# Kernel optimization log

Measured on AMD Instinct MI355X. Metric: run time of the kernel, lower is better.

Reference implementation:

```python
import jax, jax.numpy as jnp
import numpy as np

V = 50000      # word vocab
CV = 63        # char vocab (60 chars + 3 tags)
HW = 512       # word hidden size
HC = 256       # char hidden size
NLW = 2        # word lstm layers
NLC = 2        # char lstm layers
L = 12         # chars in the word


def _lstm_layers(x, H, C, Wih, Whh, bih, bhh):
    """One time-step of a multi-layer LSTM (PyTorch gate order i,f,g,o).
    x: [1, D], H/C: [nl, 1, D]. Returns (top_h, newH, newC)."""
    nl = Wih.shape[0]
    newH, newC = [], []
    inp = x
    for l in range(nl):
        gates = inp @ Wih[l].T + H[l] @ Whh[l].T + bih[l] + bhh[l]  # [1, 4D]
        i, f, g, o = jnp.split(gates, 4, axis=-1)
        i = jax.nn.sigmoid(i)
        f = jax.nn.sigmoid(f)
        g = jnp.tanh(g)
        o = jax.nn.sigmoid(o)
        c = f * C[l] + i * g
        h = o * jnp.tanh(c)
        newH.append(h)
        newC.append(c)
        inp = h
    return inp, jnp.stack(newH), jnp.stack(newC)


def setup_inputs() -> dict:
    key = jax.random.key(0)
    ks = jax.random.split(key, 20)
    sW = 1.0 / np.sqrt(HW)
    sC = 1.0 / np.sqrt(HC)
    return {
        "x_word": jax.random.randint(ks[0], (1,), 0, V),
        "x_char": jax.random.randint(ks[1], (L,), 0, CV),
        "h_word_h": jax.random.normal(ks[2], (NLW, 1, HW), jnp.float32),
        "h_word_c": jax.random.normal(ks[3], (NLW, 1, HW), jnp.float32),
        "h_char_h": jax.random.normal(ks[4], (NLC, 1, HC), jnp.float32),
        "h_char_c": jax.random.normal(ks[5], (NLC, 1, HC), jnp.float32),
        "word_emb": jax.random.normal(ks[6], (V, HW), jnp.float32),
        "word_Wih": jax.random.normal(ks[7], (NLW, 4 * HW, HW), jnp.float32) * sW,
        "word_Whh": jax.random.normal(ks[8], (NLW, 4 * HW, HW), jnp.float32) * sW,
        "word_bih": jax.random.normal(ks[9], (NLW, 4 * HW), jnp.float32) * sW,
        "word_bhh": jax.random.normal(ks[10], (NLW, 4 * HW), jnp.float32) * sW,
        "dec_W": jax.random.normal(ks[11], (V, HW), jnp.float32) * sW,
        "dec_b": jax.random.normal(ks[12], (V,), jnp.float32) * sW,
        "char_emb": jax.random.normal(ks[13], (CV, HC), jnp.float32),
        "char_Wih": jax.random.normal(ks[14], (NLC, 4 * HC, HC), jnp.float32) * sC,
        "char_Whh": jax.random.normal(ks[15], (NLC, 4 * HC, HC), jnp.float32) * sC,
        "char_bih": jax.random.normal(ks[16], (NLC, 4 * HC), jnp.float32) * sC,
        "char_bhh": jax.random.normal(ks[17], (NLC, 4 * HC), jnp.float32) * sC,
        "char_to_embedding": jax.random.normal(ks[18], (HW, HC), jnp.float32),
        "g_w": jax.random.normal(ks[19], (HW,), jnp.float32) * sW,
        "g_b": jax.random.normal(jax.random.fold_in(key, 99), (1,), jnp.float32),
    }


def reference(x_word, x_char, h_word_h, h_word_c, h_char_h, h_char_c,
              word_emb, word_Wih, word_Whh, word_bih, word_bhh,
              dec_W, dec_b,
              char_emb, char_Wih, char_Whh, char_bih, char_bhh,
              char_to_embedding, g_w, g_b):
    # character-level recurrence over the word's characters
    def char_step(carry, cidx):
        H, C = carry
        xc = char_emb[cidx][None, :]  # [1, HC]
        _, H, C = _lstm_layers(xc, H, C, char_Wih, char_Whh, char_bih, char_bhh)
        return (H, C), None

    (h_char_h, h_char_c), _ = jax.lax.scan(char_step, (h_char_h, h_char_c), x_char)

    # note: original uses h_char[1] (the CELL state) of the last layer
    x_c = char_to_embedding @ h_char_c[-1].T          # [HW, 1]
    x_w = word_emb[x_word[0]][None, :]                # [1, HW]
    g = jax.nn.relu(jnp.dot(g_w, x_w[0]) + g_b[0])    # scalar gate
    x = (1.0 - g) * x_w + g * x_c.T                   # [1, HW]

    y, h_word_h, h_word_c = _lstm_layers(x, h_word_h, h_word_c,
                                         word_Wih, word_Whh, word_bih, word_bhh)
    y = y @ dec_W.T + dec_b                           # [1, V]
    return y, h_word_h, h_word_c, h_char_h, h_char_c
```

## Files before the change

kernel.cpp:

```cpp
#include <hip/hip_runtime.h>
#include <stdint.h>


#define SCOPE_AGT __HIP_MEMORY_SCOPE_AGENT

#define CNT_CHAR   0
#define CNT_CDONE  64
#define CNT_MIX    128
#define CNT_W0     192
#define CNT_W1     256

static __device__ __forceinline__ float dot4(float4 w, const float* p){
    return w.x*p[0] + w.y*p[1] + w.z*p[2] + w.w*p[3];
}
static __device__ __forceinline__ float dot44(float4 a, float4 b){
    return a.x*b.x + a.y*b.y + a.z*b.z + a.w*b.w;
}
static __device__ __forceinline__ float sigf(float x){ return 1.0f / (1.0f + __expf(-x)); }
static __device__ __forceinline__ float tanhf_(float x){
    x = fminf(fmaxf(x, -15.0f), 15.0f);
    float e = __expf(2.0f * x);
    return (e - 1.0f) / (e + 1.0f);
}

static __device__ __forceinline__ float gload(const float* p){
    return __hip_atomic_load(p, __ATOMIC_RELAXED, SCOPE_AGT);
}
static __device__ __forceinline__ void gstore(float* p, float v){
    __hip_atomic_store(p, v, __ATOMIC_RELAXED, SCOPE_AGT);
}
static __device__ __forceinline__ void bar_add(int* c){
    __hip_atomic_fetch_add(c, 1, __ATOMIC_RELAXED, SCOPE_AGT);
}
static __device__ __forceinline__ void bar_wait_fast(int* c, int tgt){
    while (__hip_atomic_load(c, __ATOMIC_RELAXED, SCOPE_AGT) < tgt)
        __builtin_amdgcn_s_sleep(2);
}
static __device__ __forceinline__ void bar_wait_slow(int* c, int tgt){
    while (__hip_atomic_load(c, __ATOMIC_RELAXED, SCOPE_AGT) < tgt)
        __builtin_amdgcn_s_sleep(64);
}

static __device__ __forceinline__ void dec_prefetch(const float* __restrict__ dec_W,
        int start, int stride, int lane){
    float acc[8] = {0.f,0.f,0.f,0.f,0.f,0.f,0.f,0.f};
    for (int r = start; r < 50000; r += 8*stride){
        #pragma unroll
        for (int k = 0; k < 8; ++k){
            int rr = r + k * stride;
            if (rr < 50000) acc[k] += dec_W[(size_t)rr * 512 + lane * 8];
        }
    }
    float s = acc[0]+acc[1]+acc[2]+acc[3]+acc[4]+acc[5]+acc[6]+acc[7];
    asm volatile("" :: "v"(s));
}

__global__ __launch_bounds__(256, 2) void k_fused(
    const int* __restrict__ x_word, const int* __restrict__ x_char,
    const float* __restrict__ hwh, const float* __restrict__ hwc,
    const float* __restrict__ hch, const float* __restrict__ hcc,
    const float* __restrict__ word_emb,
    const float* __restrict__ wWih, const float* __restrict__ wWhh,
    const float* __restrict__ wbih, const float* __restrict__ wbhh,
    const float* __restrict__ dec_W, const float* __restrict__ dec_b,
    const float* __restrict__ char_emb,
    const float* __restrict__ cWih, const float* __restrict__ cWhh,
    const float* __restrict__ cbih, const float* __restrict__ cbhh,
    const float* __restrict__ cte,
    const float* __restrict__ g_w, const float* __restrict__ g_b,
    float* __restrict__ ws, float* __restrict__ out)
{
    const int tid  = threadIdx.x;
    const int bx   = blockIdx.x;
    const int lane = tid & 63;
    const int wv   = tid >> 6;
    int* cnt = (int*)(ws + 4096);

    if (bx < 64){
        __shared__ float sH1[256], sH2[256], sE[256], sg1[16], sg2[16];
        float* h1b = ws;
        float* h2b = ws + 512;

        const int rg = tid >> 4, lane16 = tid & 15;
        const int gate = rg & 3, uu = rg >> 2;
        const int u = (bx << 2) + uu;
        const int row = (gate << 8) + u, row2 = 1024 + row;

        float4 w1i[4], w1h[4], w2i[4], w2h[4];
        {
            const float4* p1i = (const float4*)(cWih + (size_t)row  * 256) + lane16 * 4;
            const float4* p1h = (const float4*)(cWhh + (size_t)row  * 256) + lane16 * 4;
            const float4* p2i = (const float4*)(cWih + (size_t)row2 * 256) + lane16 * 4;
            const float4* p2h = (const float4*)(cWhh + (size_t)row2 * 256) + lane16 * 4;
            #pragma unroll
            for (int j = 0; j < 4; ++j){ w1i[j]=p1i[j]; w1h[j]=p1h[j]; w2i[j]=p2i[j]; w2h[j]=p2h[j]; }
        }
        const float b1 = cbih[row]  + cbhh[row];
        const float b2 = cbih[row2] + cbhh[row2];

        float c1r = 0.f, c2r = 0.f, h1fin = 0.f, h2fin = 0.f;
        if (tid < 4)      c1r = hcc[(bx<<2) + tid];
        else if (tid < 8) c2r = hcc[256 + (bx<<2) + (tid-4)];

        for (int t = 0; t <= 12; ++t){
            sH1[tid] = (t == 0) ? hch[tid] : gload(h1b + (t & 1)*256 + tid);
            if (t >= 1) sH2[tid] = (t == 1) ? hch[256 + tid]
                                            : gload(h2b + ((t-1) & 1)*256 + tid);
            if (t < 12) sE[tid] = char_emb[x_char[t]*256 + tid];
            __syncthreads();

            float a1 = 0.f, a2 = 0.f;
            if (t < 12){
                const float* xp = sE  + lane16*16;
                const float* hp = sH1 + lane16*16;
                #pragma unroll
                for (int j = 0; j < 4; ++j) a1 += dot4(w1i[j], xp + 4*j) + dot4(w1h[j], hp + 4*j);
            }
            if (t >= 1){
                const float* xp = sH1 + lane16*16;
                const float* hp = sH2 + lane16*16;
                #pragma unroll
                for (int j = 0; j < 4; ++j) a2 += dot4(w2i[j], xp + 4*j) + dot4(w2h[j], hp + 4*j);
            }
            #pragma unroll
            for (int m = 8; m >= 1; m >>= 1){
                a1 += __shfl_xor(a1, m, 64);
                a2 += __shfl_xor(a2, m, 64);
            }
            if (lane16 == 0){
                if (t < 12) sg1[rg] = a1 + b1;
                if (t >= 1) sg2[rg] = a2 + b2;
            }
            __syncthreads();

            if (tid < 4){
                if (t < 12){
                    int uh = (bx << 2) + tid;
                    float gi = sigf(sg1[tid*4+0]);
                    float gf = sigf(sg1[tid*4+1]);
                    float gg = tanhf_(sg1[tid*4+2]);
                    float go = sigf(sg1[tid*4+3]);
                    float c = gf * c1r + gi * gg;
                    c1r = c;
                    float h = go * tanhf_(c);
                    h1fin = h;
                    gstore(h1b + ((t+1) & 1)*256 + uh, h);
                }
            } else if (tid < 8){
                if (t >= 1){
                    int q = tid - 4;
                    int uh = (bx << 2) + q;
                    float gi = sigf(sg2[q*4+0]);
                    float gf = sigf(sg2[q*4+1]);
                    float gg = tanhf_(sg2[q*4+2]);
                    float go = sigf(sg2[q*4+3]);
                    float c = gf * c2r + gi * gg;
                    c2r = c;
                    float h = go * tanhf_(c);
                    h2fin = h;
                    if (t < 12) gstore(h2b + (t & 1)*256 + uh, h);
                    else        gstore(ws + 1280 + uh, c);
                }
            }
            __syncthreads();
            if (tid == 0){
                bar_add(&cnt[CNT_CHAR]);
                if (t < 12) bar_wait_fast(&cnt[CNT_CHAR], 64*(t+1));
            }
            __syncthreads();
        }
        if (tid == 0) bar_add(&cnt[CNT_CDONE]);

        if (tid < 4){
            int uh = (bx << 2) + tid;
            out[52048 + uh] = h1fin;
            out[52560 + uh] = c1r;
        } else if (tid < 8){
            int uh = (bx << 2) + (tid - 4);
            out[52048 + 256 + uh] = h2fin;
            out[52560 + 256 + uh] = c2r;
        }

    } else if (bx < 192){
        __shared__ float sC2[256];
        __shared__ float sXCW[512];
        __shared__ float sMisc[8];
        const int vw = ((bx - 64) << 2) + wv;
        float4 wi0[4], wi1[4], wh0[4], wh1[4]; float bs[4];
        #pragma unroll
        for (int gq = 0; gq < 4; ++gq){
            const size_t rf = (size_t)((gq << 9) + vw);
            const float4* pi = (const float4*)(wWih + rf*512) + lane*2;
            const float4* ph = (const float4*)(wWhh + rf*512) + lane*2;
            wi0[gq] = pi[0]; wi1[gq] = pi[1];
            wh0[gq] = ph[0]; wh1[gq] = ph[1];
            bs[gq] = wbih[rf] + wbhh[rf];
        }
        const float4* hv = (const float4*)(hwh) + lane*2;
        const float4 hva = hv[0], hvb = hv[1];
        const size_t wbase = (size_t)x_word[0] * 512;
        const float4* wep = (const float4*)(word_emb + wbase) + lane*2;
        const float4 wea = wep[0], web = wep[1];

        if (bx == 64){
            float p = g_w[2*tid]   * word_emb[wbase + 2*tid]
                    + g_w[2*tid+1] * word_emb[wbase + 2*tid+1];
            #pragma unroll
            for (int m = 32; m >= 1; m >>= 1) p += __shfl_xor(p, m, 64);
            if (lane == 0) sMisc[wv] = p;
            __syncthreads();
            if (tid == 0)
                gstore(ws + 3072, fmaxf(sMisc[0]+sMisc[1]+sMisc[2]+sMisc[3] + g_b[0], 0.0f));
        }

        dec_prefetch(dec_W, ((bx - 64) << 2) + wv, 1024, lane);

        if (tid == 0) bar_wait_slow(&cnt[CNT_CDONE], 64);
        __syncthreads();
        sC2[tid] = gload(ws + 1280 + tid);
        __syncthreads();

        {
            float4 cv  = ((const float4*)(cte + (size_t)vw*256))[lane];
            float4 c2v = ((const float4*)sC2)[lane];
            float acc = dot44(cv, c2v);
            #pragma unroll
            for (int m = 32; m >= 1; m >>= 1) acc += __shfl_xor(acc, m, 64);
            if (lane == 0) gstore(ws + 1536 + vw, acc);
        }
        __syncthreads();
        if (tid == 0){ bar_add(&cnt[CNT_MIX]); bar_wait_fast(&cnt[CNT_MIX], 128); }
        __syncthreads();
        sXCW[tid]       = gload(ws + 1536 + tid);
        sXCW[256 + tid] = gload(ws + 1536 + 256 + tid);
        if (tid == 0) sMisc[4] = gload(ws + 3072);
        __syncthreads();

        {
            const float g  = sMisc[4];
            const float og = 1.0f - g;
            const float4 x0 = ((const float4*)sXCW)[lane*2];
            const float4 x1 = ((const float4*)sXCW)[lane*2 + 1];
            float4 xa, xb;
            xa.x = og*wea.x + g*x0.x; xa.y = og*wea.y + g*x0.y;
            xa.z = og*wea.z + g*x0.z; xa.w = og*wea.w + g*x0.w;
            xb.x = og*web.x + g*x1.x; xb.y = og*web.y + g*x1.y;
            xb.z = og*web.z + g*x1.z; xb.w = og*web.w + g*x1.w;
            float ac[4];
            #pragma unroll
            for (int gq = 0; gq < 4; ++gq){
                float a = dot44(wi0[gq], xa) + dot44(wi1[gq], xb)
                        + dot44(wh0[gq], hva) + dot44(wh1[gq], hvb);
                #pragma unroll
                for (int m = 32; m >= 1; m >>= 1) a += __shfl_xor(a, m, 64);
                ac[gq] = a;
            }
            if (lane == 0){
                float gi = sigf(ac[0] + bs[0]);
                float gf = sigf(ac[1] + bs[1]);
                float gg = tanhf_(ac[2] + bs[2]);
                float go = sigf(ac[3] + bs[3]);
                float c = gf * hwc[vw] + gi * gg;
                float h = go * tanhf_(c);
                gstore(ws + 2048 + vw, h);
                out[50000 + vw] = h;
                out[51024 + vw] = c;
            }
        }
        __syncthreads();
        if (tid == 0) bar_add(&cnt[CNT_W0]);

    } else {
        __shared__ float sX1[512];
        const int vw = ((bx - 192) << 2) + wv;
        float4 wi0[4], wi1[4], wh0[4], wh1[4]; float bs[4];
        #pragma unroll
        for (int gq = 0; gq < 4; ++gq){
            const size_t rf = (size_t)(2048 + (gq << 9) + vw);
            const float4* pi = (const float4*)(wWih + rf*512) + lane*2;
            const float4* ph = (const float4*)(wWhh + rf*512) + lane*2;
            wi0[gq] = pi[0]; wi1[gq] = pi[1];
            wh0[gq] = ph[0]; wh1[gq] = ph[1];
            bs[gq] = wbih[rf] + wbhh[rf];
        }
        const float4* hv = (const float4*)(hwh + 512) + lane*2;
        const float4 hva = hv[0], hvb = hv[1];

        dec_prefetch(dec_W, 512 + ((bx - 192) << 2) + wv, 1024, lane);

        if (tid == 0) bar_wait_slow(&cnt[CNT_W0], 128);
        __syncthreads();
        sX1[tid]       = gload(ws + 2048 + tid);
        sX1[256 + tid] = gload(ws + 2048 + 256 + tid);
        __syncthreads();
        {
            const float4 xa = ((const float4*)sX1)[lane*2];
            const float4 xb = ((const float4*)sX1)[lane*2 + 1];
            float ac[4];
            #pragma unroll
            for (int gq = 0; gq < 4; ++gq){
                float a = dot44(wi0[gq], xa) + dot44(wi1[gq], xb)
                        + dot44(wh0[gq], hva) + dot44(wh1[gq], hvb);
                #pragma unroll
                for (int m = 32; m >= 1; m >>= 1) a += __shfl_xor(a, m, 64);
                ac[gq] = a;
            }
            if (lane == 0){
                float gi = sigf(ac[0] + bs[0]);
                float gf = sigf(ac[1] + bs[1]);
                float gg = tanhf_(ac[2] + bs[2]);
                float go = sigf(ac[3] + bs[3]);
                float c = gf * hwc[512 + vw] + gi * gg;
                float h = go * tanhf_(c);
                gstore(ws + 2560 + vw, h);
                out[50000 + 512 + vw] = h;
                out[51024 + 512 + vw] = c;
            }
        }
        __syncthreads();
        if (tid == 0) bar_add(&cnt[CNT_W1]);
    }

    __shared__ float sHW[512];
    if (tid == 0) bar_wait_slow(&cnt[CNT_W1], 128);
    __syncthreads();
    sHW[tid]       = gload(ws + 2560 + tid);
    sHW[256 + tid] = gload(ws + 2560 + 256 + tid);
    __syncthreads();
    {
        const float4 ha = ((const float4*)sHW)[lane*2];
        const float4 hb = ((const float4*)sHW)[lane*2 + 1];
        const int wid = (bx << 2) + wv;
        int r = wid;
        float4 a0 = make_float4(0,0,0,0), b0 = a0;
        if (r < 50000){
            const float4* wp = (const float4*)(dec_W + (size_t)r*512) + lane*2;
            a0 = wp[0]; b0 = wp[1];
        }
        while (r < 50000){
            const int rn = r + 1280;
            float4 a1 = make_float4(0,0,0,0), b1 = a1;
            if (rn < 50000){
                const float4* wp = (const float4*)(dec_W + (size_t)rn*512) + lane*2;
                a1 = wp[0]; b1 = wp[1];
            }
            float acc = dot44(a0, ha) + dot44(b0, hb);
            #pragma unroll
            for (int m = 32; m >= 1; m >>= 1) acc += __shfl_xor(acc, m, 64);
            if (lane == 0) out[r] = acc + dec_b[r];
            r = rn; a0 = a1; b0 = b1;
        }
    }
}

extern "C" void kernel_launch(void* const* d_in, const int* in_sizes, int n_in,
                              void* d_out, int out_size, void* d_ws, size_t ws_size,
                              hipStream_t stream)
{
    const int*   x_word   = (const int*)d_in[0];
    const int*   x_char   = (const int*)d_in[1];
    const float* hwh      = (const float*)d_in[2];
    const float* hwc      = (const float*)d_in[3];
    const float* hch      = (const float*)d_in[4];
    const float* hcc      = (const float*)d_in[5];
    const float* word_emb = (const float*)d_in[6];
    const float* wWih     = (const float*)d_in[7];
    const float* wWhh     = (const float*)d_in[8];
    const float* wbih     = (const float*)d_in[9];
    const float* wbhh     = (const float*)d_in[10];
    const float* dec_W    = (const float*)d_in[11];
    const float* dec_b    = (const float*)d_in[12];
    const float* char_emb = (const float*)d_in[13];
    const float* cWih     = (const float*)d_in[14];
    const float* cWhh     = (const float*)d_in[15];
    const float* cbih     = (const float*)d_in[16];
    const float* cbhh     = (const float*)d_in[17];
    const float* cte      = (const float*)d_in[18];
    const float* g_w      = (const float*)d_in[19];
    const float* g_b      = (const float*)d_in[20];

    float* ws  = (float*)d_ws;
    float* out = (float*)d_out;

    hipMemsetAsync((void*)((char*)d_ws + 16384), 0, 2048, stream);

    hipLaunchKernelGGL(k_fused, dim3(320), dim3(256), 0, stream,
        x_word, x_char, hwh, hwc, hch, hcc, word_emb,
        wWih, wWhh, wbih, wbhh, dec_W, dec_b,
        char_emb, cWih, cWhh, cbih, cbhh, cte, g_w, g_b,
        ws, out);
}
```

Measured before the change: 331.0 us.

## Replace atomic-counter barriers with per-block flags and widen decoder GEMV per wave

Global atomic-counter barriers between the char LSTM steps and word LSTM stages are replaced by per-block sequence flags polled by a full wavefront using ballot. Char-layer hidden states are exchanged through packed per-block slots read with 64-bit loads. The decoder projection now processes 8 rows per wave with 8 lanes per row and deeper unrolled loads, reducing shuffle-reduction overhead. This aims to cut barrier latency in the serial recurrence and to improve memory-level parallelism in the bandwidth-bound decoder. The cost is more polling traffic and relaxed-ordering assumptions on the flag/data visibility.

```diff
diff --git a/kernel.cpp b/kernel.cpp
--- a/kernel.cpp
+++ b/kernel.cpp
@@ -3,12 +3,7 @@
 
 
 #define SCOPE_AGT __HIP_MEMORY_SCOPE_AGENT
-
-#define CNT_CHAR   0
-#define CNT_CDONE  64
-#define CNT_MIX    128
-#define CNT_W0     192
-#define CNT_W1     256
+#define ALL64 0xFFFFFFFFFFFFFFFFull
 
 static __device__ __forceinline__ float dot4(float4 w, const float* p){
     return w.x*p[0] + w.y*p[1] + w.z*p[2] + w.w*p[3];
@@ -29,16 +24,17 @@
 static __device__ __forceinline__ void gstore(float* p, float v){
     __hip_atomic_store(p, v, __ATOMIC_RELAXED, SCOPE_AGT);
 }
-static __device__ __forceinline__ void bar_add(int* c){
-    __hip_atomic_fetch_add(c, 1, __ATOMIC_RELAXED, SCOPE_AGT);
-}
-static __device__ __forceinline__ void bar_wait_fast(int* c, int tgt){
-    while (__hip_atomic_load(c, __ATOMIC_RELAXED, SCOPE_AGT) < tgt)
-        __builtin_amdgcn_s_sleep(2);
-}
-static __device__ __forceinline__ void bar_wait_slow(int* c, int tgt){
-    while (__hip_atomic_load(c, __ATOMIC_RELAXED, SCOPE_AGT) < tgt)
-        __builtin_amdgcn_s_sleep(64);
+static __device__ __forceinline__ int gload_i(const int* p){
+    return __hip_atomic_load(p, __ATOMIC_RELAXED, SCOPE_AGT);
+}
+static __device__ __forceinline__ void gstore_i(int* p, int v){
+    __hip_atomic_store(p, v, __ATOMIC_RELAXED, SCOPE_AGT);
+}
+static __device__ __forceinline__ unsigned long long gload_ll(const float* p){
+    return __hip_atomic_load((const unsigned long long*)p, __ATOMIC_RELAXED, SCOPE_AGT);
+}
+static __device__ __forceinline__ unsigned long long gload_ll_i(const int* p){
+    return __hip_atomic_load((const unsigned long long*)p, __ATOMIC_RELAXED, SCOPE_AGT);
 }
 
 static __device__ __forceinline__ void dec_prefetch(const float* __restrict__ dec_W,
@@ -74,12 +70,17 @@
     const int bx   = blockIdx.x;
     const int lane = tid & 63;
     const int wv   = tid >> 6;
-    int* cnt = (int*)(ws + 4096);
+    int*   ws_i  = (int*)(ws + 4096);
+    int*   seqf  = ws_i;
+    int*   w0f   = ws_i + 128;
+    int*   w1f   = ws_i + 256;
+    int*   cdone = ws_i + 512;
+    float* fdata = ws + 4864;
+
+    __shared__ float sHW[512];
 
     if (bx < 64){
         __shared__ float sH1[256], sH2[256], sE[256], sg1[16], sg2[16];
-        float* h1b = ws;
-        float* h2b = ws + 512;
 
         const int rg = tid >> 4, lane16 = tid & 15;
         const int gate = rg & 3, uu = rg >> 2;
@@ -103,9 +104,31 @@
         else if (tid < 8) c2r = hcc[256 + (bx<<2) + (tid-4)];
 
         for (int t = 0; t <= 12; ++t){
-            sH1[tid] = (t == 0) ? hch[tid] : gload(h1b + (t & 1)*256 + tid);
-            if (t >= 1) sH2[tid] = (t == 1) ? hch[256 + tid]
-                                            : gload(h2b + ((t-1) & 1)*256 + tid);
+            if (t == 0){
+                sH1[tid] = hch[tid];
+            } else {
+                if (t == 1) sH2[tid] = hch[256 + tid];
+                if (tid < 64){
+                    const int p = (t - 1) & 1;
+                    const int* sq = seqf + p*64;
+                    while (true){
+                        int v = gload_i(sq + tid);
+                        if (__ballot(v >= t) == ALL64) break;
+                    }
+                    const float* dl = fdata + (size_t)(p*64 + tid)*16;
+                    union { unsigned long long u; float f[2]; } q0,q1,q2,q3;
+                    q0.u = gload_ll(dl + 0);
+                    q1.u = gload_ll(dl + 2);
+                    q2.u = gload_ll(dl + 4);
+                    q3.u = gload_ll(dl + 6);
+                    sH1[4*tid+0] = q0.f[0]; sH1[4*tid+1] = q0.f[1];
+                    sH1[4*tid+2] = q1.f[0]; sH1[4*tid+3] = q1.f[1];
+                    if (t >= 2){
+                        sH2[4*tid+0] = q2.f[0]; sH2[4*tid+1] = q2.f[1];
+                        sH2[4*tid+2] = q3.f[0]; sH2[4*tid+3] = q3.f[1];
+                    }
+                }
+            }
             if (t < 12) sE[tid] = char_emb[x_char[t]*256 + tid];
             __syncthreads();
 
@@ -133,9 +156,10 @@
             }
             __syncthreads();
 
+            const int p2 = t & 1;
+            float* dst = fdata + (size_t)(p2*64 + bx)*16;
             if (tid < 4){
                 if (t < 12){
-                    int uh = (bx << 2) + tid;
                     float gi = sigf(sg1[tid*4+0]);
                     float gf = sigf(sg1[tid*4+1]);
                     float gg = tanhf_(sg1[tid*4+2]);
@@ -144,12 +168,11 @@
                     c1r = c;
                     float h = go * tanhf_(c);
                     h1fin = h;
-                    gstore(h1b + ((t+1) & 1)*256 + uh, h);
+                    gstore(dst + tid, h);
                 }
             } else if (tid < 8){
                 if (t >= 1){
                     int q = tid - 4;
-                    int uh = (bx << 2) + q;
                     float gi = sigf(sg2[q*4+0]);
                     float gf = sigf(sg2[q*4+1]);
                     float gg = tanhf_(sg2[q*4+2]);
@@ -158,18 +181,13 @@
                     c2r = c;
                     float h = go * tanhf_(c);
                     h2fin = h;
-                    if (t < 12) gstore(h2b + (t & 1)*256 + uh, h);
-                    else        gstore(ws + 1280 + uh, c);
+                    if (t < 12) gstore(dst + 4 + q, h);
+                    else        gstore(ws + 1280 + (bx<<2) + q, c);
                 }
             }
             __syncthreads();
-            if (tid == 0){
-                bar_add(&cnt[CNT_CHAR]);
-                if (t < 12) bar_wait_fast(&cnt[CNT_CHAR], 64*(t+1));
-            }
-            __syncthreads();
-        }
-        if (tid == 0) bar_add(&cnt[CNT_CDONE]);
+            if (tid == 0) gstore_i(seqf + p2*64 + bx, t + 1);
+        }
 
         if (tid < 4){
             int uh = (bx << 2) + tid;
@@ -179,6 +197,14 @@
             int uh = (bx << 2) + (tid - 4);
             out[52048 + 256 + uh] = h2fin;
             out[52560 + 256 + uh] = c2r;
+        }
+
+        if (bx == 0 && tid < 64){
+            while (true){
+                int v = gload_i(seqf + tid);
+                if (__ballot(v >= 13) == ALL64) break;
+            }
+            if (tid == 0) gstore_i(cdone, 1);
         }
 
     } else if (bx < 192){
@@ -215,7 +241,7 @@
 
         dec_prefetch(dec_W, ((bx - 64) << 2) + wv, 1024, lane);
 
-        if (tid == 0) bar_wait_slow(&cnt[CNT_CDONE], 64);
+        if (tid == 0){ while (gload_i(cdone) < 1) __builtin_amdgcn_s_sleep(8); }
         __syncthreads();
         sC2[tid] = gload(ws + 1280 + tid);
         __syncthreads();
@@ -229,7 +255,14 @@
             if (lane == 0) gstore(ws + 1536 + vw, acc);
         }
         __syncthreads();
-        if (tid == 0){ bar_add(&cnt[CNT_MIX]); bar_wait_fast(&cnt[CNT_MIX], 128); }
+        if (tid == 0) gstore_i(w0f + (bx - 64), 1);
+        if (tid < 64){
+            while (true){
+                unsigned long long v = gload_ll_i(w0f + 2*tid);
+                int lo = (int)(v & 0xffffffffu), hi = (int)(v >> 32);
+                if (__ballot(lo >= 1 && hi >= 1) == ALL64) break;
+            }
+        }
         __syncthreads();
         sXCW[tid]       = gload(ws + 1536 + tid);
         sXCW[256 + tid] = gload(ws + 1536 + 256 + tid);
@@ -268,7 +301,7 @@
             }
         }
         __syncthreads();
-        if (tid == 0) bar_add(&cnt[CNT_W0]);
+        if (tid == 0) gstore_i(w0f + (bx - 64), 2);
 
     } else {
         __shared__ float sX1[512];
@@ -288,7 +321,14 @@
 
         dec_prefetch(dec_W, 512 + ((bx - 192) << 2) + wv, 1024, lane);
 
-        if (tid == 0) bar_wait_slow(&cnt[CNT_W0], 128);
+        if (tid < 64){
+            while (true){
+                unsigned long long v = gload_ll_i(w0f + 2*tid);
+                int lo = (int)(v & 0xffffffffu), hi = (int)(v >> 32);
+                if (__ballot(lo >= 2 && hi >= 2) == ALL64) break;
+                __builtin_amdgcn_s_sleep(2);
+            }
+        }
         __syncthreads();
         sX1[tid]       = gload(ws + 2048 + tid);
         sX1[256 + tid] = gload(ws + 2048 + 256 + tid);
@@ -318,37 +358,42 @@
             }
         }
         __syncthreads();
-        if (tid == 0) bar_add(&cnt[CNT_W1]);
+        if (tid == 0) gstore_i(w1f + (bx - 192), 1);
     }
 
-    __shared__ float sHW[512];
-    if (tid == 0) bar_wait_slow(&cnt[CNT_W1], 128);
+    if (tid < 64){
+        while (true){
+            unsigned long long v = gload_ll_i(w1f + 2*tid);
+            int lo = (int)(v & 0xffffffffu), hi = (int)(v >> 32);
+            if (__ballot(lo >= 1 && hi >= 1) == ALL64) break;
+            __builtin_amdgcn_s_sleep(4);
+        }
+    }
     __syncthreads();
     sHW[tid]       = gload(ws + 2560 + tid);
     sHW[256 + tid] = gload(ws + 2560 + 256 + tid);
     __syncthreads();
     {
-        const float4 ha = ((const float4*)sHW)[lane*2];
-        const float4 hb = ((const float4*)sHW)[lane*2 + 1];
         const int wid = (bx << 2) + wv;
-        int r = wid;
-        float4 a0 = make_float4(0,0,0,0), b0 = a0;
-        if (r < 50000){
-            const float4* wp = (const float4*)(dec_W + (size_t)r*512) + lane*2;
-            a0 = wp[0]; b0 = wp[1];
-        }
-        while (r < 50000){
-            const int rn = r + 1280;
-            float4 a1 = make_float4(0,0,0,0), b1 = a1;
-            if (rn < 50000){
-                const float4* wp = (const float4*)(dec_W + (size_t)rn*512) + lane*2;
-                a1 = wp[0]; b1 = wp[1];
-            }
-            float acc = dot44(a0, ha) + dot44(b0, hb);
-            #pragma unroll
-            for (int m = 32; m >= 1; m >>= 1) acc += __shfl_xor(acc, m, 64);
-            if (lane == 0) out[r] = acc + dec_b[r];
-            r = rn; a0 = a1; b0 = b1;
+        const int rr = lane >> 3, cc = lane & 7;
+        const float4* hq = (const float4*)sHW + cc*16;
+        for (int gb = wid; gb < 6250; gb += 1280){
+            const int r = gb*8 + rr;
+            const float4* wp = (const float4*)(dec_W + (size_t)r*512 + cc*64);
+            float4 wbuf[8];
+            float acc = 0.f;
+            #pragma unroll
+            for (int j = 0; j < 8; ++j) wbuf[j] = wp[j];
+            #pragma unroll
+            for (int j = 0; j < 8; ++j) acc += dot44(wbuf[j], hq[j]);
+            #pragma unroll
+            for (int j = 0; j < 8; ++j) wbuf[j] = wp[8 + j];
+            #pragma unroll
+            for (int j = 0; j < 8; ++j) acc += dot44(wbuf[j], hq[8 + j]);
+            acc += __shfl_xor(acc, 1, 64);
+            acc += __shfl_xor(acc, 2, 64);
+            acc += __shfl_xor(acc, 4, 64);
+            if (cc == 0) out[r] = acc + dec_b[r];
         }
     }
 }
@@ -382,7 +427,7 @@
     float* ws  = (float*)d_ws;
     float* out = (float*)d_out;
 
-    hipMemsetAsync((void*)((char*)d_ws + 16384), 0, 2048, stream);
+    hipMemsetAsync((void*)((char*)d_ws + 16384), 0, 16384, stream);
 
     hipLaunchKernelGGL(k_fused, dim3(320), dim3(256), 0, stream,
         x_word, x_char, hwh, hwc, hch, hcc, word_emb,
```

After: 306.2 us. -7.5%, faster.
